# Kernel optimization log

Hardware: AMD Instinct MI355X
Metric: run time of the kernel (lower is better)

## Reference

```python
import jax, jax.numpy as jnp
import numpy as np

IN_DIM = 256
OUT_DIM = 256
BS = 8
NODE = 256
BN_EPS = 1e-5


def setup_inputs() -> dict:
    key = jax.random.key(0)
    ks = jax.random.split(key, 9)
    s_in = 1.0 / np.sqrt(IN_DIM)
    return {
        "x": jax.random.normal(ks[0], (BS, NODE, IN_DIM), dtype=jnp.float32),
        # att_proj: Linear(in_dim, out_dim)
        "Wp": jax.random.uniform(ks[1], (IN_DIM, OUT_DIM), jnp.float32, -s_in, s_in),
        "bp": jax.random.uniform(ks[2], (OUT_DIM,), jnp.float32, -s_in, s_in),
        # att_weight: (out_dim, 1) xavier_normal -> keep as (out_dim,)
        "w_att": jax.random.normal(ks[3], (OUT_DIM,), jnp.float32) * np.sqrt(2.0 / (OUT_DIM + 1)),
        # proj_with_att: Linear(in_dim, out_dim)
        "W1": jax.random.uniform(ks[4], (IN_DIM, OUT_DIM), jnp.float32, -s_in, s_in),
        "b1": jax.random.uniform(ks[5], (OUT_DIM,), jnp.float32, -s_in, s_in),
        # proj_without_att: Linear(in_dim, out_dim)
        "W2": jax.random.uniform(ks[6], (IN_DIM, OUT_DIM), jnp.float32, -s_in, s_in),
        "b2": jax.random.uniform(ks[7], (OUT_DIM,), jnp.float32, -s_in, s_in),
        # BatchNorm1d affine params
        "gamma": jnp.ones((OUT_DIM,), jnp.float32),
        "beta": jnp.zeros((OUT_DIM,), jnp.float32),
    }


def reference(x, Wp, bp, w_att, W1, b1, W2, b2, gamma, beta):
    # dropout is identity in eval mode
    # pairwise mult + att_proj fused: (b,n,m,do) = (x_n * x_m) @ Wp + bp
    h = jnp.tanh(jnp.einsum('bnd,bmd,de->bnme', x, x, Wp) + bp)
    scores = jnp.einsum('bnme,e->bnm', h, w_att)          # (b, n, m)
    att = jax.nn.softmax(scores, axis=1)                  # softmax over dim=-2 of (b,n,m,1) => axis n
    agg = jnp.einsum('bnm,bmd->bnd', att, x)              # att_map.squeeze(-1) @ x
    out = (agg @ W1 + b1) + (x @ W2 + b2)                 # dual projection
    # BatchNorm1d over flattened (bs*node) batch axis (training-mode batch stats)
    flat = out.reshape(-1, out.shape[-1])
    mean = jnp.mean(flat, axis=0)
    var = jnp.var(flat, axis=0)
    out = (out - mean) * jax.lax.rsqrt(var + BN_EPS) * gamma + beta
    return jax.nn.selu(out)
```

## Files before the change

### kernel.cpp

```cpp
#include <hip/hip_runtime.h>
#include <hip/hip_bf16.h>
#include <stdint.h>

using f32x16 = __attribute__((ext_vector_type(16))) float;
using short8 = __attribute__((ext_vector_type(8))) short;

#define C2LOG2E 2.8853900817779268f

static __device__ __forceinline__ unsigned cvt_pk_bf16(float lo, float hi) {
  unsigned r;
  asm("v_cvt_pk_bf16_f32 %0, %1, %2" : "=v"(r) : "v"(lo), "v"(hi));
  return r;
}

template <int CTRL>
static __device__ __forceinline__ float dpp_add(float v) {
  int x = __builtin_amdgcn_update_dpp(0, __float_as_int(v), CTRL, 0xF, 0xF, true);
  return v + __int_as_float(x);
}
#define DPP_XOR1 0xB1
#define DPP_XOR2 0x4E
#define DPP_XOR4 0x141
#define DPP_XOR8 0x140

__device__ static const unsigned kMagicDiv[9] = {0u, 65536u, 32768u, 21846u, 16384u,
                                                 13108u, 10923u, 9363u, 8192u};

__global__ __launch_bounds__(256) void k_prep(const float* __restrict__ x,
                                              const float* __restrict__ Wp,
                                              unsigned int* __restrict__ xfrag,
                                              unsigned int* __restrict__ wpfrag,
                                              float* __restrict__ bnacc) {
  const int bid = blockIdx.x, t = threadIdx.x;
  if (bid == 0) {
    bnacc[t] = 0.f;
    bnacc[256 + t] = 0.f;
  }
  const int half = t >> 7, dpair = (t >> 5) & 3, rc = t & 31;
  const int kk = half * 8 + dpair * 2;
  if (bid < 1024) {
    const int b = bid >> 7, mt = (bid >> 4) & 7, ks = bid & 15;
    const int m = mt * 32 + rc;
    const int k = ks * 16 + kk;
    float2 v = *(const float2*)(x + (size_t)(b * 256 + m) * 256 + k);
    xfrag[(size_t)b * 32768 + ((mt * 16 + ks) << 8) + half * 128 + rc * 4 + dpair] =
        cvt_pk_bf16(v.x, v.y);
  } else {
    const int b2 = bid - 1024;
    const int et = b2 >> 4, ks = b2 & 15;
    const int e = et * 32 + rc;
    const int k = ks * 16 + kk;
    float v0 = Wp[(size_t)k * 256 + e];
    float v1 = Wp[(size_t)(k + 1) * 256 + e];
    wpfrag[((et * 16 + ks) << 8) + half * 128 + rc * 4 + dpair] = cvt_pk_bf16(v0, v1);
  }
}

__global__ __launch_bounds__(512, 2) void k_scores(
    const unsigned int* __restrict__ xfrag, const unsigned int* __restrict__ wpfrag,
    const float* __restrict__ bp, const float* __restrict__ watt,
    float* __restrict__ sp) {
  __shared__ unsigned char wplds[131072];

  const int tid = threadIdx.x;
  const int l = tid & 63, w = tid >> 6;
  const int c = l & 31, hi = l >> 5;

  {
    const unsigned char* src = (const unsigned char*)wpfrag;
    #pragma unroll
    for (int it = 0; it < 16; ++it) {
      __builtin_amdgcn_global_load_lds(
          (const __attribute__((address_space(1))) unsigned int*)(src + it * 8192 + w * 1024 + l * 16),
          (__attribute__((address_space(3))) unsigned int*)(&wplds[it * 8192 + w * 1024]),
          16, 0, 0);
    }
  }

  float bpe[8], wm2[8], Wl = 0.f;
  #pragma unroll
  for (int et = 0; et < 8; ++et) {
    float bv = bp[et * 32 + c];
    float wv = watt[et * 32 + c];
    bpe[et] = bv * C2LOG2E;
    wm2[et] = -2.f * wv;
    Wl += wv;
  }
  __syncthreads();

  const int gw = blockIdx.x * 8 + w;

  for (int i = gw; i < 9216; i += 2048) {
    int b = i / 1152;
    int r = i - b * 1152;
    int nt, cum;
    if      (r < 256)  { nt = 0; cum = 0; }
    else if (r < 480)  { nt = 1; cum = 256; }
    else if (r < 672)  { nt = 2; cum = 480; }
    else if (r < 832)  { nt = 3; cum = 672; }
    else if (r < 960)  { nt = 4; cum = 832; }
    else if (r < 1056) { nt = 5; cum = 960; }
    else               { nt = (r < 1120) ? 6 : 7; cum = (r < 1120) ? 1056 : 1120; }
    int rr = r - cum;
    int w8 = 8 - nt;
    int q0 = (int)(((unsigned)rr * kMagicDiv[w8]) >> 16);
    int n  = nt * 32 + q0;
    int mt = nt + (rr - q0 * w8);
    const int m0 = mt * 32;

    const unsigned char* xfb = (const unsigned char*)xfrag + (size_t)b * 131072;
    const unsigned char* xnbase = xfb + (nt << 14) + hi * 512 + q0 * 16;
    const unsigned char* xmbase = xfb + (mt << 14) + l * 16;

    f32x16 acc[8];
    #pragma unroll
    for (int et = 0; et < 8; ++et)
      #pragma unroll
      for (int q = 0; q < 16; ++q) acc[et][q] = 0.f;

    #pragma unroll 2
    for (int ks = 0; ks < 16; ++ks) {
      uint4 xnp = *(const uint4*)(xnbase + (ks << 10));
      uint4 xm  = *(const uint4*)(xmbase + (ks << 10));
      union U { uint4 u; short8 s; __hip_bfloat162 hh[4]; } a, mm, nn;
      mm.u = xm; nn.u = xnp;
      #pragma unroll
      for (int d = 0; d < 4; ++d) a.hh[d] = __hmul2(mm.hh[d], nn.hh[d]);

      #pragma unroll
      for (int et = 0; et < 8; ++et) {
        short8 bf = *(const short8*)(&wplds[((et * 16 + ks) << 10) + l * 16]);
        acc[et] = __builtin_amdgcn_mfma_f32_32x32x16_bf16(a.s, bf, acc[et], 0, 0, 0);
      }
    }

    float p[16];
    #pragma unroll
    for (int q = 0; q < 16; ++q) {
      float pq = Wl;
      #pragma unroll
      for (int et = 0; et < 8; ++et) {
        float v = fmaf(acc[et][q], C2LOG2E, bpe[et]);
        pq = fmaf(wm2[et], __builtin_amdgcn_rcpf(1.f + exp2f(v)), pq);
      }
      p[q] = pq;
    }

    #pragma unroll
    for (int q = 0; q < 16; ++q) {
      float v = p[q];
      v = dpp_add<DPP_XOR1>(v);
      v = dpp_add<DPP_XOR2>(v);
      v = dpp_add<DPP_XOR4>(v);
      v = dpp_add<DPP_XOR8>(v);
      v += __shfl_xor(v, 16);
      p[q] = v;
    }
    if (c == 0) {
      float* outrow = sp + (size_t)(b * 256 + n) * 256 + m0;
      #pragma unroll
      for (int q = 0; q < 16; ++q) {
        int mr = (q & 3) + 8 * (q >> 2) + 4 * hi;
        outrow[mr] = p[q];
      }
      if (mt > nt) {
        #pragma unroll
        for (int q = 0; q < 16; ++q) {
          int mr = (q & 3) + 8 * (q >> 2) + 4 * hi;
          sp[(size_t)(b * 256 + m0 + mr) * 256 + n] = p[q];
        }
      }
    }
  }
}

__global__ __launch_bounds__(256) void k_colstats(const float* __restrict__ sp,
                                                  float* __restrict__ colM,
                                                  float* __restrict__ colInv) {
  __shared__ float tile[256][33];
  __shared__ float red[8][32];
  const int t = threadIdx.x;
  const int bb = blockIdx.x >> 3, mt = blockIdx.x & 7;
  const int m0 = mt * 32;
  const int col = t & 31, g = t >> 5;

  for (int cc = 0; cc < 32; ++cc) {
    int nn = cc * 8 + g;
    tile[nn][col] = sp[(size_t)(bb * 256 + nn) * 256 + m0 + col];
  }
  __syncthreads();
  float mx = -1e30f;
  for (int k2 = 0; k2 < 32; ++k2) mx = fmaxf(mx, tile[g * 32 + k2][col]);
  red[g][col] = mx;
  __syncthreads();
  float M = red[0][col];
  #pragma unroll
  for (int j = 1; j < 8; ++j) M = fmaxf(M, red[j][col]);
  float sm = 0.f;
  for (int k2 = 0; k2 < 32; ++k2) sm += __expf(tile[g * 32 + k2][col] - M);
  __syncthreads();
  red[g][col] = sm;
  __syncthreads();
  if (g == 0) {
    float S = red[0][col];
    #pragma unroll
    for (int j = 1; j < 8; ++j) S += red[j][col];
    colM[bb * 256 + m0 + col]   = M;
    colInv[bb * 256 + m0 + col] = 1.0f / S;
  }
}

__global__ __launch_bounds__(256) void k_aggproj(
    const float* __restrict__ x, const float* __restrict__ spRaw,
    const float* __restrict__ colM, const float* __restrict__ colInv,
    const float* __restrict__ W1, const float* __restrict__ b1,
    const float* __restrict__ W2, const float* __restrict__ b2,
    float* __restrict__ out, float* __restrict__ bnacc) {
  __shared__ float att8[8][256];
  __shared__ float xn8[8][256];
  __shared__ float agg8[8][256];
  const int t = threadIdx.x;
  const int bb = blockIdx.x >> 5, ng = blockIdx.x & 31;
  const int n0 = ng * 8;

  const float cm = colM[bb * 256 + t];
  const float ci = colInv[bb * 256 + t];
  #pragma unroll
  for (int i = 0; i < 8; ++i) {
    float s = spRaw[(size_t)(bb * 256 + n0 + i) * 256 + t];
    att8[i][t] = __expf(s - cm) * ci;
    xn8[i][t]  = x[(size_t)(bb * 256 + n0 + i) * 256 + t];
  }
  __syncthreads();

  float ar[8] = {0.f, 0.f, 0.f, 0.f, 0.f, 0.f, 0.f, 0.f};
  for (int m4 = 0; m4 < 64; ++m4) {
    int m = m4 * 4;
    float xv0 = x[(size_t)(bb * 256 + m + 0) * 256 + t];
    float xv1 = x[(size_t)(bb * 256 + m + 1) * 256 + t];
    float xv2 = x[(size_t)(bb * 256 + m + 2) * 256 + t];
    float xv3 = x[(size_t)(bb * 256 + m + 3) * 256 + t];
    #pragma unroll
    for (int i = 0; i < 8; ++i) {
      float4 av = *(const float4*)&att8[i][m];
      ar[i] += av.x * xv0 + av.y * xv1 + av.z * xv2 + av.w * xv3;
    }
  }
  #pragma unroll
  for (int i = 0; i < 8; ++i) agg8[i][t] = ar[i];
  __syncthreads();

  float o[8];
  float bsum = b1[t] + b2[t];
  #pragma unroll
  for (int i = 0; i < 8; ++i) o[i] = bsum;
  for (int d4 = 0; d4 < 64; ++d4) {
    int d = d4 * 4;
    float w10 = W1[(d + 0) * 256 + t], w11 = W1[(d + 1) * 256 + t];
    float w12 = W1[(d + 2) * 256 + t], w13 = W1[(d + 3) * 256 + t];
    float w20 = W2[(d + 0) * 256 + t], w21 = W2[(d + 1) * 256 + t];
    float w22 = W2[(d + 2) * 256 + t], w23 = W2[(d + 3) * 256 + t];
    #pragma unroll
    for (int i = 0; i < 8; ++i) {
      float4 ag = *(const float4*)&agg8[i][d];
      float4 xn = *(const float4*)&xn8[i][d];
      o[i] += ag.x * w10 + ag.y * w11 + ag.z * w12 + ag.w * w13
            + xn.x * w20 + xn.y * w21 + xn.z * w22 + xn.w * w23;
    }
  }
  float s1 = 0.f, s2 = 0.f;
  #pragma unroll
  for (int i = 0; i < 8; ++i) {
    out[(size_t)(bb * 256 + n0 + i) * 256 + t] = o[i];
    s1 += o[i];
    s2 += o[i] * o[i];
  }
  atomicAdd(&bnacc[t], s1);
  atomicAdd(&bnacc[256 + t], s2);
}

__global__ __launch_bounds__(256) void k_bnapply(float* __restrict__ io,
                                                 const float* __restrict__ bnacc,
                                                 const float* __restrict__ gamma,
                                                 const float* __restrict__ beta) {
  const int e = threadIdx.x;
  float mean = bnacc[e] * (1.0f / 2048.0f);
  float var  = bnacc[256 + e] * (1.0f / 2048.0f) - mean * mean;
  float scl  = rsqrtf(var + 1e-5f) * gamma[e];
  float sh   = beta[e] - mean * scl;
  for (int r = blockIdx.x; r < 2048; r += gridDim.x) {
    float v = io[(size_t)r * 256 + e];
    float y = v * scl + sh;
    float s = (y > 0.f) ? 1.0507009873554805f * y
                        : 1.7580993408473766f * (__expf(y) - 1.0f);
    io[(size_t)r * 256 + e] = s;
  }
}

extern "C" void kernel_launch(void* const* d_in, const int* in_sizes, int n_in,
                              void* d_out, int out_size, void* d_ws, size_t ws_size,
                              hipStream_t stream) {
  const float* x     = (const float*)d_in[0];
  const float* Wp    = (const float*)d_in[1];
  const float* bp    = (const float*)d_in[2];
  const float* watt  = (const float*)d_in[3];
  const float* W1    = (const float*)d_in[4];
  const float* b1    = (const float*)d_in[5];
  const float* W2    = (const float*)d_in[6];
  const float* b2    = (const float*)d_in[7];
  const float* gamma = (const float*)d_in[8];
  const float* beta  = (const float*)d_in[9];
  float* out = (float*)d_out;
  float* ws  = (float*)d_ws;

  float* sp = ws;
  unsigned int* wpfragG = (unsigned int*)(ws + 524288);
  unsigned int* xfragG  = wpfragG + 32768;
  float* bnacc  = (float*)(xfragG + 262144);
  float* colM   = bnacc + 512;
  float* colInv = colM + 2048;

  k_prep    <<<1152, 256, 0, stream>>>(x, Wp, xfragG, wpfragG, bnacc);
  k_scores  <<<256,  512, 0, stream>>>(xfragG, wpfragG, bp, watt, sp);
  k_colstats<<<64,   256, 0, stream>>>(sp, colM, colInv);
  k_aggproj <<<256,  256, 0, stream>>>(x, sp, colM, colInv, W1, b1, W2, b2, out, bnacc);
  k_bnapply <<<512,  256, 0, stream>>>(out, bnacc, gamma, beta);
}
```

Before: 119.9 us.

## Fuse BatchNorm apply into aggregation kernel via cooperative grid sync

Merges the BN-apply/SELU kernel into the aggregation-projection kernel. The kernel is launched cooperatively and uses a grid-wide barrier after the atomic statistic accumulation, then normalizes the register-held outputs directly. This removes one kernel launch and the write-then-reread of the full output tensor. In exchange it adds a grid sync and a cooperative launch, which requires all 256 blocks to be co-resident.

```diff
diff --git a/kernel.cpp b/kernel.cpp
--- a/kernel.cpp
+++ b/kernel.cpp
@@ -1,6 +1,9 @@
 #include <hip/hip_runtime.h>
 #include <hip/hip_bf16.h>
+#include <hip/hip_cooperative_groups.h>
 #include <stdint.h>
+
+namespace cg = cooperative_groups;
 
 using f32x16 = __attribute__((ext_vector_type(16))) float;
 using short8 = __attribute__((ext_vector_type(8))) short;
@@ -210,12 +213,13 @@
   }
 }
 
-__global__ __launch_bounds__(256) void k_aggproj(
+__global__ __launch_bounds__(256) void k_aggbn(
     const float* __restrict__ x, const float* __restrict__ spRaw,
     const float* __restrict__ colM, const float* __restrict__ colInv,
     const float* __restrict__ W1, const float* __restrict__ b1,
     const float* __restrict__ W2, const float* __restrict__ b2,
-    float* __restrict__ out, float* __restrict__ bnacc) {
+    float* __restrict__ out, float* __restrict__ bnacc,
+    const float* __restrict__ gamma, const float* __restrict__ beta) {
   __shared__ float att8[8][256];
   __shared__ float xn8[8][256];
   __shared__ float agg8[8][256];
@@ -270,30 +274,23 @@
   }
   float s1 = 0.f, s2 = 0.f;
   #pragma unroll
-  for (int i = 0; i < 8; ++i) {
-    out[(size_t)(bb * 256 + n0 + i) * 256 + t] = o[i];
-    s1 += o[i];
-    s2 += o[i] * o[i];
-  }
+  for (int i = 0; i < 8; ++i) { s1 += o[i]; s2 += o[i] * o[i]; }
   atomicAdd(&bnacc[t], s1);
   atomicAdd(&bnacc[256 + t], s2);
-}
-
-__global__ __launch_bounds__(256) void k_bnapply(float* __restrict__ io,
-                                                 const float* __restrict__ bnacc,
-                                                 const float* __restrict__ gamma,
-                                                 const float* __restrict__ beta) {
-  const int e = threadIdx.x;
-  float mean = bnacc[e] * (1.0f / 2048.0f);
-  float var  = bnacc[256 + e] * (1.0f / 2048.0f) - mean * mean;
-  float scl  = rsqrtf(var + 1e-5f) * gamma[e];
-  float sh   = beta[e] - mean * scl;
-  for (int r = blockIdx.x; r < 2048; r += gridDim.x) {
-    float v = io[(size_t)r * 256 + e];
-    float y = v * scl + sh;
+
+  __threadfence();
+  cg::this_grid().sync();
+
+  float mean = bnacc[t] * (1.0f / 2048.0f);
+  float var  = bnacc[256 + t] * (1.0f / 2048.0f) - mean * mean;
+  float scl  = rsqrtf(var + 1e-5f) * gamma[t];
+  float sh   = beta[t] - mean * scl;
+  #pragma unroll
+  for (int i = 0; i < 8; ++i) {
+    float y = o[i] * scl + sh;
     float s = (y > 0.f) ? 1.0507009873554805f * y
                         : 1.7580993408473766f * (__expf(y) - 1.0f);
-    io[(size_t)r * 256 + e] = s;
+    out[(size_t)(bb * 256 + n0 + i) * 256 + t] = s;
   }
 }
 
@@ -323,6 +320,9 @@
   k_prep    <<<1152, 256, 0, stream>>>(x, Wp, xfragG, wpfragG, bnacc);
   k_scores  <<<256,  512, 0, stream>>>(xfragG, wpfragG, bp, watt, sp);
   k_colstats<<<64,   256, 0, stream>>>(sp, colM, colInv);
-  k_aggproj <<<256,  256, 0, stream>>>(x, sp, colM, colInv, W1, b1, W2, b2, out, bnacc);
-  k_bnapply <<<512,  256, 0, stream>>>(out, bnacc, gamma, beta);
-}
+
+  void* args[] = {(void*)&x, (void*)&sp, (void*)&colM, (void*)&colInv,
+                  (void*)&W1, (void*)&b1, (void*)&W2, (void*)&b2,
+                  (void*)&out, (void*)&bnacc, (void*)&gamma, (void*)&beta};
+  hipLaunchCooperativeKernel((void*)k_aggbn, dim3(256), dim3(256), args, 0, stream);
+}
```

Measured after the change: 158.4 us. 1.32x slower.
